# Kernel optimization log

Hardware: AMD Instinct MI355X
Metric: run time of the kernel (lower is better)

## Reference

```python
import jax, jax.numpy as jnp
import numpy as np

B, S, D = 2, 2048, 1024
N, M, HD = 16, 4, 64          # query heads, kv heads, head dim
G = N // M                    # GQA group size
V = 32000
GIN = 12                      # gate input dim
ROPE_THETA = 1024.0
ROT = int(HD * 0.5)           # partial rotary dim = 32
EPS = 1e-6
STD = 0.006


def setup_inputs() -> dict:
    key = jax.random.key(0)
    ks = jax.random.split(key, 10)
    tn = lambda k, shape: (STD * jax.random.truncated_normal(k, -3, 3, shape)).astype(jnp.float32)
    return {
        "x": jax.random.normal(ks[0], (B, S, D), jnp.float32),
        "token_ids": jax.random.randint(ks[1], (B, S), 0, V),
        "mask": jnp.tril(jnp.ones((S, S), dtype=bool)),  # causal
        "w_q": tn(ks[2], (D, N * HD)),
        "w_k": tn(ks[3], (D, M * HD)),
        "w_v": tn(ks[4], (D, M * HD)),
        "w_o": tn(ks[5], (N * HD, D)),  # zeros at init; random for a meaningful baseline
        "ve_embed": tn(ks[6], (V, M * HD)),
        "value_lambda": jnp.full((), 0.5, jnp.float32),
        "ve_lambda": jnp.full((), 0.5, jnp.float32),
        "ve_gate": tn(ks[7], (GIN, M)),
        "attn_gate": tn(ks[8], (GIN, N)),
    }


def _qk_norm(t):
    var = jnp.mean(jnp.square(t.astype(jnp.float32)), axis=-1, keepdims=True)
    return (t * jax.lax.rsqrt(var + EPS)).astype(t.dtype)


def _rope(t):
    # partial rotary: rotate first ROT dims only
    half = ROT // 2
    inv_freq = 1.0 / ROPE_THETA ** (jnp.arange(half, dtype=jnp.float32) / half)
    ang = jnp.arange(S, dtype=jnp.float32)[:, None] * inv_freq[None, :]
    cos = jnp.cos(ang)[None, :, None, :]  # [1,S,1,half]
    sin = jnp.sin(ang)[None, :, None, :]
    rot, pas = t[..., :ROT], t[..., ROT:]
    x1, x2 = jnp.split(rot, 2, axis=-1)
    return jnp.concatenate([x1 * cos - x2 * sin, x2 * cos + x1 * sin, pas], axis=-1)


def reference(x, token_ids, mask, w_q, w_k, w_v, w_o, ve_embed,
              value_lambda, ve_lambda, ve_gate, attn_gate):
    q = (x @ w_q).reshape(B, S, N, HD)
    k = (x @ w_k).reshape(B, S, M, HD)
    v = (x @ w_v).reshape(B, S, M, HD)
    q = _rope(_qk_norm(q))
    k = _rope(_qk_norm(k))

    # value-embedding lambda mixing with sigmoid gate
    ve = ve_embed[token_ids].reshape(B, S, M, HD)
    ve_g = 2.0 * jax.nn.sigmoid(x[..., :GIN] @ ve_gate)       # [B,S,M]
    v = value_lambda * v + ve_lambda * ve_g[..., None] * ve

    # GQA causal attention (group q heads over kv heads, no kv repeat)
    qg = q.reshape(B, S, M, G, HD)
    scale = 1.0 / np.sqrt(HD).astype(np.float32)
    scores = jnp.einsum('bqmgd,bkmd->bmgqk', qg, k) * scale   # [B,M,G,S,S]
    scores = jnp.where(mask[None, None, None], scores, jnp.float32(-1e30))
    p = jax.nn.softmax(scores, axis=-1)
    attn = jnp.einsum('bmgqk,bkmd->bqmgd', p, v).reshape(B, S, N, HD)

    # output sigmoid gate then out-projection
    a_g = 2.0 * jax.nn.sigmoid(x[..., :GIN] @ attn_gate)      # [B,S,N]
    attn = a_g[..., None] * attn
    return attn.reshape(B, S, N * HD) @ w_o
```

## Files before the change

kernel.cpp:

```cpp
#include <hip/hip_runtime.h>
#include <math.h>

#define S_LEN 2048
#define NHEADS 16
#define KVH 4

typedef __attribute__((ext_vector_type(8))) _Float16 half8;
typedef __attribute__((ext_vector_type(4))) _Float16 half4;
typedef __attribute__((ext_vector_type(2))) __fp16 fp16x2;
typedef __attribute__((ext_vector_type(4))) float f32x4;

__device__ inline void gld16(const void* g, void* l) {
  __builtin_amdgcn_global_load_lds(
      (const __attribute__((address_space(1))) unsigned int*)g,
      (__attribute__((address_space(3))) unsigned int*)l, 16, 0, 0);
}

__global__ __launch_bounds__(256) void setup_fused(
    const float* __restrict__ wq, const float* __restrict__ wk,
    const float* __restrict__ wv, const float* __restrict__ wo,
    const float* __restrict__ x, const float* __restrict__ attn_gate,
    _Float16* __restrict__ wqkvT, _Float16* __restrict__ woT,
    float2* __restrict__ costab, float* __restrict__ ag,
    _Float16* __restrict__ xh)
{
  const int t = threadIdx.x;
  int L = blockIdx.x;

  if (L >= 1024) {
    const size_t i = ((size_t)(L - 1024) * 256 + t) * 16;
    #pragma unroll
    for (int c = 0; c < 2; c++) {
      float4 f0 = *(const float4*)(x + i + c * 8);
      float4 f1 = *(const float4*)(x + i + c * 8 + 4);
      half8 h;
      h[0] = (_Float16)f0.x; h[1] = (_Float16)f0.y; h[2] = (_Float16)f0.z; h[3] = (_Float16)f0.w;
      h[4] = (_Float16)f1.x; h[5] = (_Float16)f1.y; h[6] = (_Float16)f1.z; h[7] = (_Float16)f1.w;
      *(half8*)(xh + i + c * 8) = h;
    }
    return;
  }
  if (L >= 768) {
    const int row = (L - 768) * 16 + (t >> 4);
    const int n = t & 15;
    float z = 0.f;
    #pragma unroll
    for (int i = 0; i < 12; ++i) z += x[(size_t)row * 1024 + i] * attn_gate[i * NHEADS + n];
    ag[(size_t)row * NHEADS + n] = 2.f / (1.f + __expf(-z));
    return;
  }
  if (L >= 640) {
    const int gi = (L - 640) * 256 + t;
    const int s = gi >> 4, i = gi & 15;
    const float ang = (float)s * exp2f(-0.625f * (float)i);
    float c, sn;
    sincosf(ang, &sn, &c);
    costab[gi] = make_float2(c, sn);
    return;
  }

  const float* in; _Float16* out; int C, ct, rt;
  if (L < 256)      { in = wq; out = wqkvT;                       C = 1024; ct = (L & 15) * 64; rt = (L >> 4) * 64; }
  else if (L < 320) { L -= 256; in = wk; out = wqkvT + (size_t)1024 * 1024; C = 256; ct = (L & 3) * 64; rt = (L >> 2) * 64; }
  else if (L < 384) { L -= 320; in = wv; out = wqkvT + (size_t)1280 * 1024; C = 256; ct = (L & 3) * 64; rt = (L >> 2) * 64; }
  else              { L -= 384; in = wo; out = woT;               C = 1024; ct = (L & 15) * 64; rt = (L >> 4) * 64; }

  __shared__ float Ls[64][65];
  {
    const int r = t >> 2, cs = (t & 3) << 4;
    const float* src = in + (size_t)(rt + r) * C + ct + cs;
    #pragma unroll
    for (int j = 0; j < 16; j += 4) {
      float4 v = *(const float4*)(src + j);
      Ls[r][cs + j] = v.x; Ls[r][cs + j + 1] = v.y;
      Ls[r][cs + j + 2] = v.z; Ls[r][cs + j + 3] = v.w;
    }
  }
  __syncthreads();
  {
    const int c = t >> 2, rs = (t & 3) << 4;
    half8 h0, h1;
    #pragma unroll
    for (int j = 0; j < 8; j++) h0[j] = (_Float16)Ls[rs + j][c];
    #pragma unroll
    for (int j = 0; j < 8; j++) h1[j] = (_Float16)Ls[rs + 8 + j][c];
    _Float16* dst = out + (size_t)(ct + c) * 1024 + rt + rs;
    *(half8*)dst = h0;
    *(half8*)(dst + 8) = h1;
  }
}

template<typename OUT_T, bool EPI>
__global__ __launch_bounds__(256) void gemm_k(
    const _Float16* __restrict__ A, const _Float16* __restrict__ BT,
    OUT_T* __restrict__ C, int M, int N, int K, int lda,
    const float2* __restrict__ costab)
{
  __shared__ _Float16 lds[12288];
  const int t = threadIdx.x;
  const int w = t >> 6, l = t & 63;
  const int lg = l >> 4, ll = l & 15;
  const int bm = blockIdx.y * 64, bn = blockIdx.x * 128;
  const int wr = (w >> 1) * 32, wc = (w & 1) * 64;
  const int srow = t >> 2, sslot = t & 3;

  f32x4 acc[2][4] = {};

  auto stage = [&](int k0, int buf) {
    char* Ab = (char*)lds + buf * 4096;
    char* Bb = (char*)lds + 8192 + buf * 8192;
    const int so = (sslot ^ (srow & 3)) << 3;
    gld16(A  + (size_t)(bm + srow)      * lda + k0 + so, Ab + w * 1024);
    gld16(BT + (size_t)(bn + srow)      * K   + k0 + so, Bb + w * 1024);
    gld16(BT + (size_t)(bn + srow + 64) * K   + k0 + so, Bb + 4096 + w * 1024);
  };

  stage(0, 0);
  __syncthreads();

  int buf = 0;
  for (int k0 = 0; k0 < K; k0 += 32) {
    if (k0 + 32 < K) stage(k0 + 32, buf ^ 1);

    const char* Ab = (const char*)lds + buf * 4096;
    const char* Bb = (const char*)lds + 8192 + buf * 8192;
    half8 af[2], bfr[4];
    #pragma unroll
    for (int mt = 0; mt < 2; mt++) {
      const int row = wr + mt * 16 + ll;
      af[mt] = *(const half8*)(Ab + row * 64 + ((lg ^ (row & 3)) << 4));
    }
    #pragma unroll
    for (int nt = 0; nt < 4; nt++) {
      const int row = wc + nt * 16 + ll;
      bfr[nt] = *(const half8*)(Bb + row * 64 + ((lg ^ (row & 3)) << 4));
    }
    __builtin_amdgcn_s_setprio(1);
    #pragma unroll
    for (int mt = 0; mt < 2; mt++)
      #pragma unroll
      for (int nt = 0; nt < 4; nt++)
        acc[mt][nt] = __builtin_amdgcn_mfma_f32_16x16x32_f16(af[mt], bfr[nt], acc[mt][nt], 0, 0, 0);
    __builtin_amdgcn_s_setprio(0);

    __syncthreads();
    buf ^= 1;
  }

  if constexpr (EPI) {
    const int col0 = bn + wc;
    const int head = col0 >> 6;
    const bool isv = head >= 20;
    const float qs = (head < 16) ? 0.18033688f : 1.0f;
    #pragma unroll
    for (int mt = 0; mt < 2; mt++) {
      if (isv) {
        #pragma unroll
        for (int r = 0; r < 4; r++) {
          const size_t row = (size_t)bm + wr + mt * 16 + lg * 4 + r;
          #pragma unroll
          for (int nt = 0; nt < 4; nt++)
            C[row * N + col0 + nt * 16 + ll] = (OUT_T)acc[mt][nt][r];
        }
      } else {
        float ss[4];
        #pragma unroll
        for (int r = 0; r < 4; r++)
          ss[r] = acc[mt][0][r] * acc[mt][0][r] + acc[mt][1][r] * acc[mt][1][r]
                + acc[mt][2][r] * acc[mt][2][r] + acc[mt][3][r] * acc[mt][3][r];
        #pragma unroll
        for (int mi = 0; mi < 4; mi++) {
          const int msk = 1 << mi;
          #pragma unroll
          for (int r = 0; r < 4; r++) ss[r] += __shfl_xor(ss[r], msk);
        }
        #pragma unroll
        for (int r = 0; r < 4; r++) {
          const size_t row = (size_t)bm + wr + mt * 16 + lg * 4 + r;
          const float inv = rsqrtf(ss[r] * (1.0f / 64.0f) + 1e-6f) * qs;
          const float2 cs2 = costab[(row & (S_LEN - 1)) * 16 + ll];
          const float a0 = acc[mt][0][r] * inv, a1 = acc[mt][1][r] * inv;
          C[row * N + col0 +      ll] = (OUT_T)(a0 * cs2.x - a1 * cs2.y);
          C[row * N + col0 + 16 + ll] = (OUT_T)(a1 * cs2.x + a0 * cs2.y);
          C[row * N + col0 + 32 + ll] = (OUT_T)(acc[mt][2][r] * inv);
          C[row * N + col0 + 48 + ll] = (OUT_T)(acc[mt][3][r] * inv);
        }
      }
    }
  } else {
    #pragma unroll
    for (int mt = 0; mt < 2; mt++) {
      #pragma unroll
      for (int r = 0; r < 4; r++) {
        const size_t row = (size_t)bm + wr + mt * 16 + lg * 4 + r;
        #pragma unroll
        for (int nt = 0; nt < 4; nt++) {
          const int col = bn + wc + nt * 16 + ll;
          if constexpr (sizeof(OUT_T) == 2) C[row * N + col] = (OUT_T)(_Float16)acc[mt][nt][r];
          else                              C[row * N + col] = acc[mt][nt][r];
        }
      }
    }
  }
}

__global__ __launch_bounds__(256) void vtrans_mix(
    const _Float16* __restrict__ qkv, const float* __restrict__ x,
    const int* __restrict__ token_ids, const float* __restrict__ ve_embed,
    const float* __restrict__ ve_gate, const float* __restrict__ vlam,
    const float* __restrict__ velam, _Float16* __restrict__ vT)
{
  __shared__ _Float16 Ls[64][72];
  __shared__ float veg[64];
  __shared__ int toks[64];
  const int st = blockIdx.x * 64;
  const int bm = blockIdx.y;
  const int b = bm >> 2, m = bm & 3;
  const int t = threadIdx.x;

  if (t < 64) {
    const size_t row_g = (size_t)b * S_LEN + st + t;
    toks[t] = token_ids[row_g];
    float z = 0.f;
    #pragma unroll
    for (int i = 0; i < 12; ++i) z += x[row_g * 1024 + i] * ve_gate[i * KVH + m];
    veg[t] = velam[0] * 2.f / (1.f + __expf(-z));
  }
  __syncthreads();
  {
    const int sr = t >> 2, ds = (t & 3) << 4;
    const float vl = vlam[0];
    const _Float16* src = qkv + ((size_t)(b * S_LEN + st + sr)) * 1536 + 1280 + m * 64 + ds;
    const float* ves = ve_embed + (size_t)toks[sr] * 256 + m * 64 + ds;
    half8 v0 = *(const half8*)src;
    half8 v1 = *(const half8*)(src + 8);
    const float g = veg[sr];
    #pragma unroll
    for (int q4 = 0; q4 < 4; q4++) {
      float4 ev = *(const float4*)(ves + q4 * 4);
      const int o0 = q4 * 4;
      Ls[sr][ds + o0 + 0] = (_Float16)(vl * (float)((o0 + 0 < 8) ? v0[o0 + 0] : v1[o0 - 8]) + g * ev.x);
      Ls[sr][ds + o0 + 1] = (_Float16)(vl * (float)((o0 + 1 < 8) ? v0[o0 + 1] : v1[o0 - 7]) + g * ev.y);
      Ls[sr][ds + o0 + 2] = (_Float16)(vl * (float)((o0 + 2 < 8) ? v0[o0 + 2] : v1[o0 - 6]) + g * ev.z);
      Ls[sr][ds + o0 + 3] = (_Float16)(vl * (float)((o0 + 3 < 8) ? v0[o0 + 3] : v1[o0 - 5]) + g * ev.w);
    }
  }
  __syncthreads();
  {
    const int dr = t >> 2, ssl = (t & 3) << 4;
    half8 o0, o1;
    #pragma unroll
    for (int j = 0; j < 8; j++) { o0[j] = Ls[ssl + j][dr]; o1[j] = Ls[ssl + 8 + j][dr]; }
    _Float16* dst = vT + ((size_t)bm * 64 + dr) * S_LEN + st + ssl;
    *(half8*)dst = o0;
    *(half8*)(dst + 8) = o1;
  }
}

__global__ __launch_bounds__(256) void attn_mfma(
    _Float16* __restrict__ qkv, const _Float16* __restrict__ vT,
    const float* __restrict__ ag)
{
  const int L = blockIdx.x;
  const int qt = 31 - (L >> 5);
  const int b = (L >> 4) & 1;
  const int n = L & 15;
  const int m = n >> 2;

  const int t = threadIdx.x, w = t >> 6, l = t & 63;
  const int lg = l >> 4, ll = l & 15;

  __shared__ _Float16 lds[20480];

  const int qbase = qt * 64 + w * 16;
  const size_t qrow_g = (size_t)(b * S_LEN) + qbase;

  half8 qa[2];
  #pragma unroll
  for (int s = 0; s < 2; s++)
    qa[s] = *(const half8*)(qkv + (qrow_g + ll) * 1536 + n * 64 + s * 32 + lg * 8);

  float agr[4];
  #pragma unroll
  for (int r = 0; r < 4; r++)
    agr[r] = ag[(qrow_g + lg * 4 + r) * NHEADS + n];

  half8 ones;
  #pragma unroll
  for (int i = 0; i < 8; i++) ones[i] = (_Float16)1.0f;

  f32x4 o[4] = {};
  f32x4 ol = {};

  const int srow = l >> 3, sslot = l & 7;
  const int q_loc = w * 16 + ll;

  auto stage = [&](int kt, int buf) {
    #pragma unroll
    for (int i = 0; i < 2; i++) {
      const int kr = w * 16 + i * 8 + srow;
      const size_t kg = ((size_t)(b * S_LEN + kt * 64 + kr)) * 1536 + 1024 + m * 64
                        + ((sslot ^ (kr & 7)) << 3);
      gld16(qkv + kg, (char*)lds + buf * 8192 + w * 2048 + i * 1024);
      const int vr = w * 16 + i * 8 + srow;
      const size_t vg = ((size_t)((b * KVH + m) * 64 + vr)) * S_LEN + kt * 64
                        + ((sslot ^ (vr & 7)) << 3);
      gld16(vT + vg, (char*)lds + 16384 + buf * 8192 + w * 2048 + i * 1024);
    }
  };

  stage(0, 0);
  __syncthreads();

  for (int kt = 0; kt <= qt; kt++) {
    const int cur = kt & 1;
    if (kt < qt) stage(kt + 1, cur ^ 1);

    const char* Ksb = (const char*)lds + cur * 8192;
    const char* Vsb = (const char*)lds + 16384 + cur * 8192;
    char* Psb = (char*)lds + 32768;

    f32x4 sc[4];
    #pragma unroll
    for (int kf = 0; kf < 4; kf++) {
      sc[kf][0] = -11.6f; sc[kf][1] = -11.6f; sc[kf][2] = -11.6f; sc[kf][3] = -11.6f;
    }
    __builtin_amdgcn_s_setprio(1);
    #pragma unroll
    for (int s = 0; s < 2; s++)
      #pragma unroll
      for (int kf = 0; kf < 4; kf++) {
        const int krow = kf * 16 + ll;
        const half8 kb = *(const half8*)(Ksb + krow * 128
                          + (((4 * s + lg) ^ (krow & 7)) << 4));
        sc[kf] = __builtin_amdgcn_mfma_f32_16x16x32_f16(kb, qa[s], sc[kf], 0, 0, 0);
      }
    __builtin_amdgcn_s_setprio(0);

    if (kt == qt) {
      const int qg = qbase + ll;
      #pragma unroll
      for (int kf = 0; kf < 4; kf++)
        #pragma unroll
        for (int r = 0; r < 4; r++)
          if (kt * 64 + kf * 16 + 4 * lg + r > qg) sc[kf][r] = -1e30f;
    }

    #pragma unroll
    for (int kf = 0; kf < 4; kf++) {
      union { fp16x2 h2[2]; half4 h4; } P;
      P.h2[0] = __builtin_amdgcn_cvt_pkrtz(exp2f(sc[kf][0]), exp2f(sc[kf][1]));
      P.h2[1] = __builtin_amdgcn_cvt_pkrtz(exp2f(sc[kf][2]), exp2f(sc[kf][3]));
      const int slot = (2 * kf + (lg >> 1)) ^ (q_loc & 7);
      *(half4*)(Psb + q_loc * 128 + slot * 16 + (lg & 1) * 8) = P.h4;
    }

    __builtin_amdgcn_s_setprio(1);
    #pragma unroll
    for (int s = 0; s < 2; s++) {
      const half8 pa = *(const half8*)(Psb + q_loc * 128
                        + (((4 * s + lg) ^ (q_loc & 7)) << 4));
      ol = __builtin_amdgcn_mfma_f32_16x16x32_f16(pa, ones, ol, 0, 0, 0);
      #pragma unroll
      for (int df = 0; df < 4; df++) {
        const int vrow = df * 16 + ll;
        const half8 vb = *(const half8*)(Vsb + vrow * 128
                          + (((4 * s + lg) ^ (vrow & 7)) << 4));
        o[df] = __builtin_amdgcn_mfma_f32_16x16x32_f16(pa, vb, o[df], 0, 0, 0);
      }
    }
    __builtin_amdgcn_s_setprio(0);

    __syncthreads();
  }

  #pragma unroll
  for (int r = 0; r < 4; r++) {
    const size_t qrow = qrow_g + lg * 4 + r;
    const float scale = agr[r] / ol[r];
    #pragma unroll
    for (int df = 0; df < 4; df++)
      qkv[qrow * 1536 + n * 64 + df * 16 + ll] = (_Float16)(o[df][r] * scale);
  }
}

extern "C" void kernel_launch(void* const* d_in, const int* in_sizes, int n_in,
                              void* d_out, int out_size, void* d_ws, size_t ws_size,
                              hipStream_t stream) {
  const float* x         = (const float*)d_in[0];
  const int*   token_ids = (const int*)d_in[1];
  const float* w_q       = (const float*)d_in[3];
  const float* w_k       = (const float*)d_in[4];
  const float* w_v       = (const float*)d_in[5];
  const float* w_o       = (const float*)d_in[6];
  const float* ve_embed  = (const float*)d_in[7];
  const float* vlam      = (const float*)d_in[8];
  const float* velam     = (const float*)d_in[9];
  const float* ve_gate   = (const float*)d_in[10];
  const float* attn_gate = (const float*)d_in[11];
  float* out = (float*)d_out;

  char* p = (char*)d_ws;
  _Float16* wqkvT = (_Float16*)p; p += (size_t)1536 * 1024 * 2;
  _Float16* woT   = (_Float16*)p; p += (size_t)1024 * 1024 * 2;
  _Float16* qkv   = (_Float16*)p; p += (size_t)4096 * 1536 * 2;
  _Float16* vTb   = (_Float16*)p; p += (size_t)8 * 64 * S_LEN * 2;
  float*    ag    = (float*)p;    p += (size_t)4096 * NHEADS * 4;

  _Float16* xh = (_Float16*)d_out;
  float2* costab = (float2*)((char*)d_out + (size_t)12 * 1024 * 1024);

  dim3 blk(256);
  setup_fused<<<dim3(2048), blk, 0, stream>>>(w_q, w_k, w_v, w_o, x, attn_gate,
                                              wqkvT, woT, costab, ag, xh);

  gemm_k<_Float16, true><<<dim3(12, 64), blk, 0, stream>>>(
      xh, wqkvT, qkv, 4096, 1536, 1024, 1024, costab);

  vtrans_mix<<<dim3(32, 8), blk, 0, stream>>>(qkv, x, token_ids, ve_embed,
                                              ve_gate, vlam, velam, vTb);

  attn_mfma<<<dim3(1024), blk, 0, stream>>>(qkv, vTb, ag);

  gemm_k<float, false><<<dim3(8, 64), blk, 0, stream>>>(
      qkv, woT, out, 4096, 1024, 1024, 1536, nullptr);
}
```

Baseline: 98.52 us.

## Split attention key tile across warp pairs with 32-row query fragments

Each warp now handles 32 query rows against half of the 64-key tile (split-K within the block), instead of 16 query rows against all 64 keys. Each K and V fragment read from LDS now feeds two MFMAs, halving LDS read traffic per MFMA. The two key halves are combined at the end through an LDS reduction of partial outputs and row sums. This costs more accumulator registers and an extra sync plus reduction at the epilogue.

New measurement: 95.80 us. 2.8% less time.

```diff
diff --git a/kernel.cpp b/kernel.cpp
--- a/kernel.cpp
+++ b/kernel.cpp
@@ -269,31 +269,38 @@
 
   const int t = threadIdx.x, w = t >> 6, l = t & 63;
   const int lg = l >> 4, ll = l & 15;
+  const int g  = w & 1;
+  const int kh = w >> 1;
 
   __shared__ _Float16 lds[20480];
 
-  const int qbase = qt * 64 + w * 16;
-  const size_t qrow_g = (size_t)(b * S_LEN) + qbase;
-
-  half8 qa[2];
+  const int qbl = qt * 64 + g * 32;
+  const size_t qrow_g = (size_t)(b * S_LEN) + qbl;
+
+  half8 qa[2][2];
   #pragma unroll
-  for (int s = 0; s < 2; s++)
-    qa[s] = *(const half8*)(qkv + (qrow_g + ll) * 1536 + n * 64 + s * 32 + lg * 8);
-
-  float agr[4];
-  #pragma unroll
-  for (int r = 0; r < 4; r++)
-    agr[r] = ag[(qrow_g + lg * 4 + r) * NHEADS + n];
+  for (int qf = 0; qf < 2; qf++)
+    #pragma unroll
+    for (int s = 0; s < 2; s++)
+      qa[qf][s] = *(const half8*)(qkv + (qrow_g + qf * 16 + ll) * 1536 + n * 64 + s * 32 + lg * 8);
+
+  float agr[2][4];
+  if (kh == 0) {
+    #pragma unroll
+    for (int qf = 0; qf < 2; qf++)
+      #pragma unroll
+      for (int r = 0; r < 4; r++)
+        agr[qf][r] = ag[(qrow_g + qf * 16 + lg * 4 + r) * NHEADS + n];
+  }
 
   half8 ones;
   #pragma unroll
   for (int i = 0; i < 8; i++) ones[i] = (_Float16)1.0f;
 
-  f32x4 o[4] = {};
-  f32x4 ol = {};
+  f32x4 o[2][4] = {};
+  f32x4 ol[2] = {};
 
   const int srow = l >> 3, sslot = l & 7;
-  const int q_loc = w * 16 + ll;
 
   auto stage = [&](int kt, int buf) {
     #pragma unroll
@@ -320,53 +327,69 @@
     const char* Vsb = (const char*)lds + 16384 + cur * 8192;
     char* Psb = (char*)lds + 32768;
 
-    f32x4 sc[4];
-    #pragma unroll
-    for (int kf = 0; kf < 4; kf++) {
-      sc[kf][0] = -11.6f; sc[kf][1] = -11.6f; sc[kf][2] = -11.6f; sc[kf][3] = -11.6f;
-    }
+    f32x4 sc[2][2];
+    #pragma unroll
+    for (int qf = 0; qf < 2; qf++)
+      #pragma unroll
+      for (int kf = 0; kf < 2; kf++) {
+        sc[qf][kf][0] = -11.6f; sc[qf][kf][1] = -11.6f;
+        sc[qf][kf][2] = -11.6f; sc[qf][kf][3] = -11.6f;
+      }
     __builtin_amdgcn_s_setprio(1);
     #pragma unroll
     for (int s = 0; s < 2; s++)
       #pragma unroll
-      for (int kf = 0; kf < 4; kf++) {
-        const int krow = kf * 16 + ll;
+      for (int kf = 0; kf < 2; kf++) {
+        const int krow = kh * 32 + kf * 16 + ll;
         const half8 kb = *(const half8*)(Ksb + krow * 128
                           + (((4 * s + lg) ^ (krow & 7)) << 4));
-        sc[kf] = __builtin_amdgcn_mfma_f32_16x16x32_f16(kb, qa[s], sc[kf], 0, 0, 0);
+        sc[0][kf] = __builtin_amdgcn_mfma_f32_16x16x32_f16(kb, qa[0][s], sc[0][kf], 0, 0, 0);
+        sc[1][kf] = __builtin_amdgcn_mfma_f32_16x16x32_f16(kb, qa[1][s], sc[1][kf], 0, 0, 0);
       }
     __builtin_amdgcn_s_setprio(0);
 
     if (kt == qt) {
-      const int qg = qbase + ll;
-      #pragma unroll
-      for (int kf = 0; kf < 4; kf++)
-        #pragma unroll
-        for (int r = 0; r < 4; r++)
-          if (kt * 64 + kf * 16 + 4 * lg + r > qg) sc[kf][r] = -1e30f;
-    }
-
-    #pragma unroll
-    for (int kf = 0; kf < 4; kf++) {
-      union { fp16x2 h2[2]; half4 h4; } P;
-      P.h2[0] = __builtin_amdgcn_cvt_pkrtz(exp2f(sc[kf][0]), exp2f(sc[kf][1]));
-      P.h2[1] = __builtin_amdgcn_cvt_pkrtz(exp2f(sc[kf][2]), exp2f(sc[kf][3]));
-      const int slot = (2 * kf + (lg >> 1)) ^ (q_loc & 7);
-      *(half4*)(Psb + q_loc * 128 + slot * 16 + (lg & 1) * 8) = P.h4;
+      #pragma unroll
+      for (int qf = 0; qf < 2; qf++) {
+        const int qg = qbl + qf * 16 + ll;
+        #pragma unroll
+        for (int kf = 0; kf < 2; kf++)
+          #pragma unroll
+          for (int r = 0; r < 4; r++)
+            if (kt * 64 + kh * 32 + kf * 16 + 4 * lg + r > qg) sc[qf][kf][r] = -1e30f;
+      }
+    }
+
+    #pragma unroll
+    for (int qf = 0; qf < 2; qf++) {
+      const int q_loc = g * 32 + qf * 16 + ll;
+      #pragma unroll
+      for (int kf = 0; kf < 2; kf++) {
+        union { fp16x2 h2[2]; half4 h4; } P;
+        P.h2[0] = __builtin_amdgcn_cvt_pkrtz(exp2f(sc[qf][kf][0]), exp2f(sc[qf][kf][1]));
+        P.h2[1] = __builtin_amdgcn_cvt_pkrtz(exp2f(sc[qf][kf][2]), exp2f(sc[qf][kf][3]));
+        const int slot = (4 * kh + 2 * kf + (lg >> 1)) ^ (q_loc & 7);
+        *(half4*)(Psb + q_loc * 128 + slot * 16 + (lg & 1) * 8) = P.h4;
+      }
     }
 
     __builtin_amdgcn_s_setprio(1);
-    #pragma unroll
-    for (int s = 0; s < 2; s++) {
-      const half8 pa = *(const half8*)(Psb + q_loc * 128
-                        + (((4 * s + lg) ^ (q_loc & 7)) << 4));
-      ol = __builtin_amdgcn_mfma_f32_16x16x32_f16(pa, ones, ol, 0, 0, 0);
+    {
+      half8 pa[2];
+      #pragma unroll
+      for (int qf = 0; qf < 2; qf++) {
+        const int prow = g * 32 + qf * 16 + ll;
+        pa[qf] = *(const half8*)(Psb + prow * 128 + (((4 * kh + lg) ^ (prow & 7)) << 4));
+      }
+      ol[0] = __builtin_amdgcn_mfma_f32_16x16x32_f16(pa[0], ones, ol[0], 0, 0, 0);
+      ol[1] = __builtin_amdgcn_mfma_f32_16x16x32_f16(pa[1], ones, ol[1], 0, 0, 0);
       #pragma unroll
       for (int df = 0; df < 4; df++) {
         const int vrow = df * 16 + ll;
         const half8 vb = *(const half8*)(Vsb + vrow * 128
-                          + (((4 * s + lg) ^ (vrow & 7)) << 4));
-        o[df] = __builtin_amdgcn_mfma_f32_16x16x32_f16(pa, vb, o[df], 0, 0, 0);
+                          + (((4 * kh + lg) ^ (vrow & 7)) << 4));
+        o[0][df] = __builtin_amdgcn_mfma_f32_16x16x32_f16(pa[0], vb, o[0][df], 0, 0, 0);
+        o[1][df] = __builtin_amdgcn_mfma_f32_16x16x32_f16(pa[1], vb, o[1][df], 0, 0, 0);
       }
     }
     __builtin_amdgcn_s_setprio(0);
@@ -374,13 +397,39 @@
     __syncthreads();
   }
 
-  #pragma unroll
-  for (int r = 0; r < 4; r++) {
-    const size_t qrow = qrow_g + lg * 4 + r;
-    const float scale = agr[r] / ol[r];
-    #pragma unroll
-    for (int df = 0; df < 4; df++)
-      qkv[qrow * 1536 + n * 64 + df * 16 + ll] = (_Float16)(o[df][r] * scale);
+  char* red = (char*)lds;
+  if (kh == 1) {
+    #pragma unroll
+    for (int qf = 0; qf < 2; qf++) {
+      #pragma unroll
+      for (int df = 0; df < 4; df++)
+        #pragma unroll
+        for (int r = 0; r < 4; r++)
+          *(float*)(red + g * 8192 + (qf * 16 + lg * 4 + r) * 256 + (df * 16 + ll) * 4)
+              = o[qf][df][r];
+      if (ll == 0)
+        #pragma unroll
+        for (int r = 0; r < 4; r++)
+          *(float*)(red + 16384 + g * 128 + (qf * 16 + lg * 4 + r) * 4) = ol[qf][r];
+    }
+  }
+  __syncthreads();
+  if (kh == 0) {
+    #pragma unroll
+    for (int qf = 0; qf < 2; qf++)
+      #pragma unroll
+      for (int r = 0; r < 4; r++) {
+        const int qloc32 = qf * 16 + lg * 4 + r;
+        const float lsum = ol[qf][r] + *(const float*)(red + 16384 + g * 128 + qloc32 * 4);
+        const size_t qrow = qrow_g + qf * 16 + lg * 4 + r;
+        const float scale = agr[qf][r] / lsum;
+        #pragma unroll
+        for (int df = 0; df < 4; df++) {
+          const float ov = o[qf][df][r]
+              + *(const float*)(red + g * 8192 + qloc32 * 256 + (df * 16 + ll) * 4);
+          qkv[qrow * 1536 + n * 64 + df * 16 + ll] = (_Float16)(ov * scale);
+        }
+      }
   }
 }
 
```
